# Kernel tuning notes

Measured on AMD Instinct MI355X. Metric: run time of the kernel, lower is better.

The kernel has to match this reference:

```python
import jax, jax.numpy as jnp
import numpy as np

S = 8    # number of path-segments
U = 32   # per-segment input width (subscript 'u')
V = 32   # per-segment output width (subscript 'v')
C = 32   # number of weight groups (indexed dimension)
Z = 65536  # number of rows


def setup_inputs() -> dict:
    key = jax.random.key(0)
    k1, k2, k3 = jax.random.split(key, 3)
    input1 = jax.random.normal(k1, (C, S * U * V), dtype=jnp.float32) * 0.05  # grouped weights
    input2 = jax.random.normal(k2, (Z, S * U), dtype=jnp.float32)             # row features
    counts = jnp.full((C,), Z // C, dtype=jnp.int32)                          # rows per group, contiguous
    coefficients = jax.random.uniform(k3, (S,), dtype=jnp.float32, minval=0.5, maxval=1.5)
    return {"input1": input1, "input2": input2, "counts": counts, "coefficients": coefficients}


def reference(input1, input2, counts, coefficients):
    # Segment-indexed grouped linear: rows are contiguous per group (sizes = counts).
    # For each path-segment s: out_s[z, v] = coeff_s * sum_u x_s[z, u] * W_s[g(z), u, v]
    # Final output concatenates the S segment outputs along the last dim.
    seg_ids = jnp.repeat(jnp.arange(C, dtype=jnp.int32), counts, total_repeat_length=Z)  # [Z]
    outs = []
    for s in range(S):
        W = input1[:, s * U * V:(s + 1) * U * V].reshape(C, U, V)  # [C,U,V]
        x = input2[:, s * U:(s + 1) * U]                           # [Z,U]
        Wz = W[seg_ids]                                            # [Z,U,V] gather by group
        outs.append(coefficients[s] * jnp.einsum('zu,zuv->zv', x, Wz))
    return jnp.concatenate(outs, axis=-1)  # [Z, S*V]
```

## Files before the change

### kernel.cpp

```cpp
#include <hip/hip_runtime.h>


constexpr int S = 8, U = 32, V = 32, C = 32, Z = 65536;
constexpr int BZ = 128;
constexpr int NT = 128;
constexpr int ZS = BZ + 4;
constexpr int WS = 36;

typedef float f4 __attribute__((ext_vector_type(4)));

__global__ __launch_bounds__(NT) void IndexedLinear_kernel(
    const float* __restrict__ W_all,
    const float* __restrict__ X,
    const int*   __restrict__ counts,
    const float* __restrict__ coeff,
    float*       __restrict__ out)
{
  const int tid = threadIdx.x;
  const int s   = blockIdx.x & 7;
  const int zb  = blockIdx.x >> 3;
  const int z0  = zb * BZ;

  __shared__ float XT[U * ZS];
  __shared__ float Wl[U * WS];
  __shared__ int   pre[C + 1];
  __shared__ int   sseg0, suni;

  if (tid <= C) {
    int a = 0;
    for (int i = 0; i < tid; ++i) a += counts[i];
    pre[tid] = a;
  }
  __syncthreads();

  if (tid == 0) {
    int a = 0, b = 0;
    #pragma unroll
    for (int i = 1; i < C; ++i) {
      if (pre[i] <= z0) a = i;
      if (pre[i] <= z0 + BZ - 1) b = i;
    }
    sseg0 = a;
    suni  = (a == b);
  }
  __syncthreads();

  const int   seg0 = sseg0;
  const int   uni  = suni;
  const float cs   = coeff[s];

  const int ug = tid & 7;
  const int zl = tid >> 3;
  f4 xv[8];
  const float* xbase = X + (size_t)z0 * (S * U) + s * U + ug * 4;
  #pragma unroll
  for (int p = 0; p < 8; ++p) {
    xv[p] = *(const f4*)(xbase + (size_t)(p * 16 + zl) * (S * U));
  }

  {
    const float* wbase = W_all + (size_t)seg0 * (S * U * V) + s * (U * V);
    #pragma unroll
    for (int k = 0; k < 2; ++k) {
      const int idx = tid + k * NT;
      f4 wv = *(const f4*)(wbase + idx * 4);
      wv *= cs;
      const int wu = idx >> 3, wc = (idx & 7) * 4;
      *(f4*)&Wl[wu * WS + wc] = wv;
    }
  }

  #pragma unroll
  for (int p = 0; p < 8; ++p) {
    const int z = p * 16 + zl;
    #pragma unroll
    for (int j = 0; j < 4; ++j) XT[(ug * 4 + j) * ZS + z] = xv[p][j];
  }
  __syncthreads();

  const int vg = tid & 7;
  const int zg = tid >> 3;
  float acc[8][4] = {};

  if (uni) {
    #pragma unroll
    for (int u = 0; u < U; ++u) {
      const f4 w  = *(const f4*)&Wl[u * WS + vg * 4];
      const f4 xa = *(const f4*)&XT[u * ZS + zg * 8];
      const f4 xb = *(const f4*)&XT[u * ZS + zg * 8 + 4];
      #pragma unroll
      for (int j = 0; j < 4; ++j) {
        #pragma unroll
        for (int i = 0; i < 4; ++i) {
          acc[i][j]     += xa[i] * w[j];
          acc[4 + i][j] += xb[i] * w[j];
        }
      }
    }
  } else {
    #pragma unroll 1
    for (int zi = 0; zi < 8; ++zi) {
      const int z = z0 + zg * 8 + zi;
      int sg = 0;
      #pragma unroll 1
      for (int i = 1; i < C; ++i) if (pre[i] <= z) sg = i;
      const float* wb = W_all + (size_t)sg * (S * U * V) + s * (U * V) + vg * 4;
      #pragma unroll 1
      for (int u = 0; u < U; ++u) {
        const float xs = XT[u * ZS + zg * 8 + zi];
        #pragma unroll
        for (int j = 0; j < 4; ++j) acc[zi][j] += xs * wb[u * V + j];
      }
      #pragma unroll
      for (int j = 0; j < 4; ++j) acc[zi][j] *= cs;
    }
  }

  float* ob = out + (size_t)(z0 + zg * 8) * (S * V) + s * V + vg * 4;
  #pragma unroll
  for (int zi = 0; zi < 8; ++zi) {
    f4 o;
    o[0] = acc[zi][0]; o[1] = acc[zi][1]; o[2] = acc[zi][2]; o[3] = acc[zi][3];
    *(f4*)(ob + (size_t)zi * (S * V)) = o;
  }
}

extern "C" void kernel_launch(void* const* d_in, const int* in_sizes, int n_in,
                              void* d_out, int out_size, void* d_ws, size_t ws_size,
                              hipStream_t stream) {
  const float* input1       = (const float*)d_in[0];
  const float* input2       = (const float*)d_in[1];
  const int*   counts       = (const int*)d_in[2];
  const float* coefficients = (const float*)d_in[3];
  float*       out          = (float*)d_out;

  const int grid = (Z / BZ) * S;
  IndexedLinear_kernel<<<grid, NT, 0, stream>>>(input1, input2, counts,
                                                coefficients, out);
}
```

Before: 128.6 us.

## Double row tile, enlarge per-thread 8x8 register tile, use wave-scan prefix

Doubles the rows per block to 256 and gives each thread an 8x8 output tile instead of 8x4, so each thread does more FMAs per shared-memory load. Replaces the serial per-thread counts prefix and the single-thread segment search with a wavefront shuffle scan and ballot/popcount. X is now loaded with nontemporal vector loads issued before the prefix computation, and the tile is transposed into shared memory with vectorized f4 stores. The cost is more accumulator registers (64) and a larger shared X tile, which can lower occupancy, and the grid is half as large.

Measured after the change: 159.8 us. 1.24x slower.

```diff
diff --git a/kernel.cpp b/kernel.cpp
--- a/kernel.cpp
+++ b/kernel.cpp
@@ -2,7 +2,7 @@
 
 
 constexpr int S = 8, U = 32, V = 32, C = 32, Z = 65536;
-constexpr int BZ = 128;
+constexpr int BZ = 256;
 constexpr int NT = 128;
 constexpr int ZS = BZ + 4;
 constexpr int WS = 36;
@@ -18,30 +18,44 @@
 {
   const int tid = threadIdx.x;
   const int s   = blockIdx.x & 7;
-  const int zb  = blockIdx.x >> 3;
-  const int z0  = zb * BZ;
+  const int z0  = (blockIdx.x >> 3) * BZ;
 
   __shared__ float XT[U * ZS];
   __shared__ float Wl[U * WS];
-  __shared__ int   pre[C + 1];
+  __shared__ int   pre[C];
   __shared__ int   sseg0, suni;
 
-  if (tid <= C) {
-    int a = 0;
-    for (int i = 0; i < tid; ++i) a += counts[i];
-    pre[tid] = a;
+  const int uq  = tid & 7;
+  const int zq4 = tid >> 3;
+  f4 xv[4][4];
+  {
+    const float* xb = X + (size_t)(z0 + zq4 * 4) * (S * U) + s * U + uq * 4;
+    #pragma unroll
+    for (int r = 0; r < 4; ++r)
+      #pragma unroll
+      for (int i = 0; i < 4; ++i)
+        xv[r][i] = __builtin_nontemporal_load(
+            (const f4*)(xb + (size_t)(r * 64 + i) * (S * U)));
   }
-  __syncthreads();
 
-  if (tid == 0) {
-    int a = 0, b = 0;
+  if (tid < 64) {
+    int c = (tid < C) ? counts[tid] : 0;
+    int inc = c;
     #pragma unroll
-    for (int i = 1; i < C; ++i) {
-      if (pre[i] <= z0) a = i;
-      if (pre[i] <= z0 + BZ - 1) b = i;
+    for (int d = 1; d < 32; d <<= 1) {
+      int o = __shfl_up(inc, d, 64);
+      if (tid >= d) inc += o;
     }
-    sseg0 = a;
-    suni  = (a == b);
+    const int exc = inc - c;
+    if (tid < C) pre[tid] = exc;
+    const unsigned long long ma = __ballot(tid < C && exc <= z0);
+    const unsigned long long mb = __ballot(tid < C && exc <= z0 + BZ - 1);
+    if (tid == 0) {
+      const int a = __popcll(ma) - 1;
+      const int b = __popcll(mb) - 1;
+      sseg0 = a;
+      suni  = (a == b);
+    }
   }
   __syncthreads();
 
@@ -49,51 +63,48 @@
   const int   uni  = suni;
   const float cs   = coeff[s];
 
-  const int ug = tid & 7;
-  const int zl = tid >> 3;
-  f4 xv[8];
-  const float* xbase = X + (size_t)z0 * (S * U) + s * U + ug * 4;
-  #pragma unroll
-  for (int p = 0; p < 8; ++p) {
-    xv[p] = *(const f4*)(xbase + (size_t)(p * 16 + zl) * (S * U));
-  }
-
   {
-    const float* wbase = W_all + (size_t)seg0 * (S * U * V) + s * (U * V);
+    const float* wb = W_all + (size_t)seg0 * (S * U * V) + s * (U * V);
     #pragma unroll
     for (int k = 0; k < 2; ++k) {
       const int idx = tid + k * NT;
-      f4 wv = *(const f4*)(wbase + idx * 4);
+      f4 wv = *(const f4*)(wb + idx * 4);
       wv *= cs;
-      const int wu = idx >> 3, wc = (idx & 7) * 4;
-      *(f4*)&Wl[wu * WS + wc] = wv;
+      *(f4*)&Wl[(idx >> 3) * WS + (idx & 7) * 4] = wv;
     }
   }
 
   #pragma unroll
-  for (int p = 0; p < 8; ++p) {
-    const int z = p * 16 + zl;
+  for (int r = 0; r < 4; ++r) {
     #pragma unroll
-    for (int j = 0; j < 4; ++j) XT[(ug * 4 + j) * ZS + z] = xv[p][j];
+    for (int j = 0; j < 4; ++j) {
+      f4 t;
+      t[0] = xv[r][0][j]; t[1] = xv[r][1][j];
+      t[2] = xv[r][2][j]; t[3] = xv[r][3][j];
+      *(f4*)&XT[(uq * 4 + j) * ZS + zq4 * 4 + r * 64] = t;
+    }
   }
   __syncthreads();
 
-  const int vg = tid & 7;
-  const int zg = tid >> 3;
-  float acc[8][4] = {};
+  const int vg = tid & 3;
+  const int zg = tid >> 2;
+  float acc[8][8] = {};
 
   if (uni) {
-    #pragma unroll
+    #pragma unroll 8
     for (int u = 0; u < U; ++u) {
-      const f4 w  = *(const f4*)&Wl[u * WS + vg * 4];
+      const f4 w0 = *(const f4*)&Wl[u * WS + vg * 8];
+      const f4 w1 = *(const f4*)&Wl[u * WS + vg * 8 + 4];
       const f4 xa = *(const f4*)&XT[u * ZS + zg * 8];
       const f4 xb = *(const f4*)&XT[u * ZS + zg * 8 + 4];
       #pragma unroll
-      for (int j = 0; j < 4; ++j) {
+      for (int i = 0; i < 4; ++i) {
         #pragma unroll
-        for (int i = 0; i < 4; ++i) {
-          acc[i][j]     += xa[i] * w[j];
-          acc[4 + i][j] += xb[i] * w[j];
+        for (int j = 0; j < 4; ++j) {
+          acc[i][j]         += xa[i] * w0[j];
+          acc[i][4 + j]     += xa[i] * w1[j];
+          acc[4 + i][j]     += xb[i] * w0[j];
+          acc[4 + i][4 + j] += xb[i] * w1[j];
         }
       }
     }
@@ -104,24 +115,26 @@
       int sg = 0;
       #pragma unroll 1
       for (int i = 1; i < C; ++i) if (pre[i] <= z) sg = i;
-      const float* wb = W_all + (size_t)sg * (S * U * V) + s * (U * V) + vg * 4;
+      const float* wb2 = W_all + (size_t)sg * (S * U * V) + s * (U * V) + vg * 8;
       #pragma unroll 1
       for (int u = 0; u < U; ++u) {
         const float xs = XT[u * ZS + zg * 8 + zi];
         #pragma unroll
-        for (int j = 0; j < 4; ++j) acc[zi][j] += xs * wb[u * V + j];
+        for (int j = 0; j < 8; ++j) acc[zi][j] += xs * wb2[u * V + j];
       }
       #pragma unroll
-      for (int j = 0; j < 4; ++j) acc[zi][j] *= cs;
+      for (int j = 0; j < 8; ++j) acc[zi][j] *= cs;
     }
   }
 
-  float* ob = out + (size_t)(z0 + zg * 8) * (S * V) + s * V + vg * 4;
+  float* ob = out + (size_t)(z0 + zg * 8) * (S * V) + s * V + vg * 8;
   #pragma unroll
   for (int zi = 0; zi < 8; ++zi) {
-    f4 o;
-    o[0] = acc[zi][0]; o[1] = acc[zi][1]; o[2] = acc[zi][2]; o[3] = acc[zi][3];
-    *(f4*)(ob + (size_t)zi * (S * V)) = o;
+    f4 o0, o1;
+    o0[0] = acc[zi][0]; o0[1] = acc[zi][1]; o0[2] = acc[zi][2]; o0[3] = acc[zi][3];
+    o1[0] = acc[zi][4]; o1[1] = acc[zi][5]; o1[2] = acc[zi][6]; o1[3] = acc[zi][7];
+    *(f4*)(ob + (size_t)zi * (S * V))     = o0;
+    *(f4*)(ob + (size_t)zi * (S * V) + 4) = o1;
   }
 }
 
```
